# Kernel tuning notes

Measured on AMD Instinct MI355X. Metric: run time of the kernel, lower is better.

The kernel has to match this reference:

```python
import jax, jax.numpy as jnp
import numpy as np

N_NODES = 50000
N_EDGES = 600000
D = 128


def _mean_agg(h, src, dst, n_nodes):
    # DGL SAGEConv 'mean': mean of incoming src features per dst node; 0 for isolated nodes
    s = jax.ops.segment_sum(h[src], dst, num_segments=n_nodes)  # [N, d]
    deg = jax.ops.segment_sum(jnp.ones_like(dst, dtype=h.dtype), dst, num_segments=n_nodes)
    return s / jnp.maximum(deg, 1.0)[:, None]


def setup_inputs() -> dict:
    key = jax.random.key(0)
    ks = jax.random.split(key, 10)
    sc = 1.0 / np.sqrt(D)
    return {
        "x": jax.random.normal(ks[0], (N_NODES, D), jnp.float32),
        "e": jax.random.normal(ks[1], (N_EDGES, D), jnp.float32),
        "src": jax.random.randint(ks[2], (N_EDGES,), 0, N_NODES, jnp.int32),
        "dst": jax.random.randint(ks[3], (N_EDGES,), 0, N_NODES, jnp.int32),
        "W1_self": jax.random.normal(ks[4], (D, D), jnp.float32) * sc,
        "W1_neigh": jax.random.normal(ks[5], (D, D), jnp.float32) * sc,
        "b1": jnp.zeros((D,), jnp.float32),
        "W2_self": jax.random.normal(ks[6], (D, D), jnp.float32) * sc,
        "W2_neigh": jax.random.normal(ks[7], (D, D), jnp.float32) * sc,
        "b2": jnp.zeros((D,), jnp.float32),
        "Wp": jax.random.normal(ks[8], (2 * D, 3), jnp.float32) * (1.0 / np.sqrt(2 * D)),
        "bp": jnp.zeros((3,), jnp.float32),
    }


def reference(x, e, src, dst, W1_self, W1_neigh, b1, W2_self, W2_neigh, b2, Wp, bp):
    n = x.shape[0]
    # SAGEConv 1 (mean) + ReLU
    agg1 = _mean_agg(x, src, dst, n)
    h = jax.nn.relu(x @ W1_self + agg1 @ W1_neigh + b1)
    # SAGEConv 2 (mean)
    agg2 = _mean_agg(h, src, dst, n)
    h = h @ W2_self + agg2 @ W2_neigh + b2
    # MLPPredictor: per-edge gather, concat, linear (edge feature e unused in score)
    he = jnp.concatenate([h[src], h[dst]], axis=1)  # [E, 2D]
    score = he @ Wp + bp  # [E, 3]
    return score
```

## Files before the change

kernel.cpp:

```cpp
#include <hip/hip_runtime.h>
#include <hip/hip_bf16.h>


typedef __attribute__((ext_vector_type(8))) short bf16x8;
typedef __attribute__((ext_vector_type(4))) float f32x4;

static __device__ __forceinline__ float bf16lo(unsigned u) {
    return __uint_as_float(u << 16);
}
static __device__ __forceinline__ float bf16hi(unsigned u) {
    return __uint_as_float(u & 0xffff0000u);
}
static __device__ __forceinline__ unsigned short f2bf(float f) {
    unsigned u = __float_as_uint(f);
    unsigned r = 0x7fffu + ((u >> 16) & 1u);
    return (unsigned short)((u + r) >> 16);
}
static __device__ __forceinline__ unsigned pack_bf162(float a, float b) {
    return (unsigned)f2bf(a) | ((unsigned)f2bf(b) << 16);
}

#define SORT_BLOCKS 256

__global__ __launch_bounds__(256) void k_misc(
    const float* __restrict__ x, unsigned short* __restrict__ xb,
    const int* __restrict__ dst, int* __restrict__ H,
    const float* __restrict__ W1s, const float* __restrict__ W1n,
    unsigned short* __restrict__ Wt1,
    const float* __restrict__ W2s, const float* __restrict__ W2n,
    const float* __restrict__ Wp, const float* __restrict__ b2,
    const float* __restrict__ bp, float* __restrict__ Wc,
    float* __restrict__ bconst, int N, int E, int CHUNK)
{
    const int nCvt = (N * 32 + 255) / 256;
    const int b = blockIdx.x;
    const int t = threadIdx.x;

    if (b < nCvt) {
        int i = b * 256 + t;
        if (i < N * 32) {
            float4 v = ((const float4*)x)[i];
            uint2 o;
            o.x = pack_bf162(v.x, v.y);
            o.y = pack_bf162(v.z, v.w);
            *(uint2*)(xb + (size_t)i * 4) = o;
        }
    } else if (b < nCvt + SORT_BLOCKS) {
        __shared__ int hist[256];
        hist[t] = 0;
        __syncthreads();
        int blk = b - nCvt;
        int start = blk * CHUNK;
        int end = min(start + CHUNK, E);
        for (int e = start + t; e < end; e += 256)
            atomicAdd(&hist[((unsigned)dst[e]) >> 8], 1);
        __syncthreads();
        H[blk * 256 + t] = hist[t];
    } else if (b < nCvt + SORT_BLOCKS + 128) {
        int id = (b - nCvt - SORT_BLOCKS) * 256 + t;
        int k = id >> 7, n = id & 127;
        float v = (k < 128) ? W1s[k * 128 + n] : W1n[(k - 128) * 128 + n];
        Wt1[n * 256 + k] = f2bf(v);
    } else {
        for (int id = t; id < 1539; id += 256) {
            if (id < 1536) {
                int c = id / 12, j = id % 12;
                int q = j / 3, jj = j % 3;
                const float* W2 = (q == 0 || q == 2) ? W2s : W2n;
                int wpoff = (q < 2) ? 0 : 128;
                float s = 0.f;
                for (int m = 0; m < 128; ++m)
                    s += W2[c * 128 + m] * Wp[(wpoff + m) * 3 + jj];
                Wc[c * 12 + j] = s;
            } else {
                int jj = id - 1536;
                float s = bp[jj];
                for (int m = 0; m < 128; ++m)
                    s += b2[m] * (Wp[m * 3 + jj] + Wp[(128 + m) * 3 + jj]);
                bconst[jj] = s;
            }
        }
    }
}

__global__ __launch_bounds__(256) void k_s2(int* __restrict__ H,
                                            int* __restrict__ bucketBase,
                                            int NB, int E) {
    const int t = threadIdx.x;
    int tot = 0;
    for (int blk = 0; blk < SORT_BLOCKS; ++blk) tot += H[blk * 256 + t];
    __shared__ int lt[256];
    lt[t] = tot;
    __syncthreads();
    for (int off = 1; off < 256; off <<= 1) {
        int u = (t >= off) ? lt[t - off] : 0;
        __syncthreads();
        lt[t] += u;
        __syncthreads();
    }
    int excl = lt[t] - tot;
    if (t < NB) bucketBase[t] = excl;
    if (t == 0) bucketBase[NB] = E;
    int run = excl;
    for (int blk = 0; blk < SORT_BLOCKS; ++blk) {
        int h = H[blk * 256 + t];
        H[blk * 256 + t] = run;
        run += h;
    }
}

__global__ __launch_bounds__(256) void k_s3(const int* __restrict__ src,
                                            const int* __restrict__ dst,
                                            const int* __restrict__ H,
                                            int* __restrict__ packed,
                                            int E, int CHUNK) {
    __shared__ int cur[256];
    const int t = threadIdx.x, blk = blockIdx.x;
    cur[t] = H[blk * 256 + t];
    __syncthreads();
    int start = blk * CHUNK, end = min(start + CHUNK, E);
    for (int e = start + t; e < end; e += 256) {
        int d = dst[e];
        int p = atomicAdd(&cur[((unsigned)d) >> 8], 1);
        packed[p] = (src[e] & 0xFFFF) | ((d & 255) << 16);
    }
}

__global__ __launch_bounds__(256) void k_s4(const int* __restrict__ packed,
                                            const int* __restrict__ bucketBase,
                                            int* __restrict__ eidx,
                                            int* __restrict__ cursor,
                                            float* __restrict__ fdeg,
                                            float* __restrict__ invdeg, int N) {
    const int t = threadIdx.x, b = blockIdx.x;
    const int rb = bucketBase[b], re = bucketBase[b + 1];
    __shared__ int cnt[256];
    __shared__ int lt[256];
    __shared__ int cur[256];
    cnt[t] = 0;
    __syncthreads();
    for (int i = rb + t; i < re; i += 256)
        atomicAdd(&cnt[(packed[i] >> 16) & 255], 1);
    __syncthreads();
    int v = cnt[t];
    lt[t] = v;
    __syncthreads();
    for (int off = 1; off < 256; off <<= 1) {
        int u = (t >= off) ? lt[t - off] : 0;
        __syncthreads();
        lt[t] += u;
        __syncthreads();
    }
    int excl = lt[t] - v;
    int node = b * 256 + t;
    if (node < N) {
        cursor[node] = rb + excl + v;
        fdeg[node] = (float)v;
        invdeg[node] = 1.0f / fmaxf((float)v, 1.0f);
    }
    cur[t] = rb + excl;
    __syncthreads();
    for (int i = rb + t; i < re; i += 256) {
        int p = packed[i];
        int pos = atomicAdd(&cur[(p >> 16) & 255], 1);
        eidx[pos] = p & 0xFFFF;
    }
}

__global__ __launch_bounds__(256) void k_gemm_fused(
    const unsigned short* __restrict__ xb,
    const int* __restrict__ eidx, const int* __restrict__ cursor,
    const float* __restrict__ fdeg, const float* __restrict__ invdeg,
    const unsigned short* __restrict__ Wt, const float* __restrict__ bias,
    const float* __restrict__ Wc, float* __restrict__ P, int N)
{
    __shared__ __align__(16) char sW[65536];
    __shared__ float sWc[1536];
    const int t = threadIdx.x;

#pragma unroll
    for (int i = 0; i < 16; ++i) {
        int o = (i * 256 + t) * 16;
        int n = o >> 9;
        int c = o & 511;
        int sw = (n << 9) | (c ^ ((n & 7) << 4));
        *(float4*)&sW[sw] = *(const float4*)((const char*)Wt + o);
    }
    for (int i = t; i < 1536; i += 256) sWc[i] = Wc[i];

    const int wave = t >> 6, lane = t & 63;
    const int nodeBase = blockIdx.x * 128 + wave * 32;
    const int lrow = lane & 15, lk = lane >> 4;
    const int r0 = nodeBase + lrow, r1 = nodeBase + 16 + lrow;

    union { bf16x8 v; unsigned u[4]; } afrag0[4], afrag1[4];

    {
        float agg[4][8];
#pragma unroll
        for (int ksb = 0; ksb < 4; ++ksb)
#pragma unroll
            for (int i = 0; i < 8; ++i) agg[ksb][i] = 0.f;
        if (r0 < N) {
            int d = (int)fdeg[r0], o = cursor[r0] - d;
            for (int j = 0; j < d; ++j) {
                int s = eidx[o + j];
                const unsigned short* row = xb + (size_t)s * 128 + lk * 8;
#pragma unroll
                for (int ksb = 0; ksb < 4; ++ksb) {
                    uint4 v = *(const uint4*)(row + ksb * 32);
                    agg[ksb][0] += bf16lo(v.x); agg[ksb][1] += bf16hi(v.x);
                    agg[ksb][2] += bf16lo(v.y); agg[ksb][3] += bf16hi(v.y);
                    agg[ksb][4] += bf16lo(v.z); agg[ksb][5] += bf16hi(v.z);
                    agg[ksb][6] += bf16lo(v.w); agg[ksb][7] += bf16hi(v.w);
                }
            }
            float sc = invdeg[r0];
#pragma unroll
            for (int ksb = 0; ksb < 4; ++ksb)
#pragma unroll
                for (int i = 0; i < 4; ++i)
                    afrag0[ksb].u[i] = pack_bf162(agg[ksb][2 * i] * sc,
                                                  agg[ksb][2 * i + 1] * sc);
        } else {
#pragma unroll
            for (int ksb = 0; ksb < 4; ++ksb)
#pragma unroll
                for (int i = 0; i < 4; ++i) afrag0[ksb].u[i] = 0u;
        }
    }
    {
        float agg[4][8];
#pragma unroll
        for (int ksb = 0; ksb < 4; ++ksb)
#pragma unroll
            for (int i = 0; i < 8; ++i) agg[ksb][i] = 0.f;
        if (r1 < N) {
            int d = (int)fdeg[r1], o = cursor[r1] - d;
            for (int j = 0; j < d; ++j) {
                int s = eidx[o + j];
                const unsigned short* row = xb + (size_t)s * 128 + lk * 8;
#pragma unroll
                for (int ksb = 0; ksb < 4; ++ksb) {
                    uint4 v = *(const uint4*)(row + ksb * 32);
                    agg[ksb][0] += bf16lo(v.x); agg[ksb][1] += bf16hi(v.x);
                    agg[ksb][2] += bf16lo(v.y); agg[ksb][3] += bf16hi(v.y);
                    agg[ksb][4] += bf16lo(v.z); agg[ksb][5] += bf16hi(v.z);
                    agg[ksb][6] += bf16lo(v.w); agg[ksb][7] += bf16hi(v.w);
                }
            }
            float sc = invdeg[r1];
#pragma unroll
            for (int ksb = 0; ksb < 4; ++ksb)
#pragma unroll
                for (int i = 0; i < 4; ++i)
                    afrag1[ksb].u[i] = pack_bf162(agg[ksb][2 * i] * sc,
                                                  agg[ksb][2 * i + 1] * sc);
        } else {
#pragma unroll
            for (int ksb = 0; ksb < 4; ++ksb)
#pragma unroll
                for (int i = 0; i < 4; ++i) afrag1[ksb].u[i] = 0u;
        }
    }

    f32x4 acc[2][8];
#pragma unroll
    for (int rs = 0; rs < 2; ++rs)
#pragma unroll
        for (int nb = 0; nb < 8; ++nb) acc[rs][nb] = (f32x4){0.f, 0.f, 0.f, 0.f};

    __syncthreads();

    for (int ks = 0; ks < 8; ++ks) {
        bf16x8 a0, a1;
        if (ks < 4) {
            const int kk = ks * 32 + lk * 8;
            a0 = (bf16x8){};
            a1 = (bf16x8){};
            if (r0 < N) a0 = *(const bf16x8*)(xb + (size_t)r0 * 128 + kk);
            if (r1 < N) a1 = *(const bf16x8*)(xb + (size_t)r1 * 128 + kk);
        } else {
            a0 = afrag0[ks - 4].v;
            a1 = afrag1[ks - 4].v;
        }
        const int cbase = ks * 64 + lk * 16;
#pragma unroll
        for (int nb = 0; nb < 8; ++nb) {
            int n = nb * 16 + lrow;
            int sw = (n << 9) | (cbase ^ ((n & 7) << 4));
            bf16x8 b = *(const bf16x8*)&sW[sw];
            acc[0][nb] = __builtin_amdgcn_mfma_f32_16x16x32_bf16(a0, b, acc[0][nb], 0, 0, 0);
            acc[1][nb] = __builtin_amdgcn_mfma_f32_16x16x32_bf16(a1, b, acc[1][nb], 0, 0, 0);
        }
    }

#pragma unroll
    for (int rs = 0; rs < 2; ++rs) {
        float hval[8][4];
#pragma unroll
        for (int nb = 0; nb < 8; ++nb) {
            float bv = bias[nb * 16 + lrow];
#pragma unroll
            for (int r = 0; r < 4; ++r)
                hval[nb][r] = fmaxf(acc[rs][nb][r] + bv, 0.f);
        }
#pragma unroll
        for (int r = 0; r < 4; ++r) {
            float pj[12];
#pragma unroll
            for (int j = 0; j < 12; ++j) pj[j] = 0.f;
#pragma unroll
            for (int nb = 0; nb < 8; ++nb) {
                float hv = hval[nb][r];
                const float* wrow = &sWc[(nb * 16 + lrow) * 12];
#pragma unroll
                for (int j = 0; j < 12; ++j) pj[j] += hv * wrow[j];
            }
#pragma unroll
            for (int off = 8; off; off >>= 1) {
#pragma unroll
                for (int j = 0; j < 12; ++j) pj[j] += __shfl_xor(pj[j], off, 64);
            }
            int node = nodeBase + rs * 16 + lk * 4 + r;
            if (lrow == 0 && node < N) {
                float* prow = &P[(size_t)node * 16];
                *(float4*)(prow + 0) = make_float4(pj[0], pj[1], pj[2], pj[3]);
                *(float4*)(prow + 4) = make_float4(pj[4], pj[5], pj[6], pj[7]);
                *(float4*)(prow + 8) = make_float4(pj[8], pj[9], pj[10], pj[11]);
            }
        }
    }
}

__global__ __launch_bounds__(256) void k_agg3(const float* __restrict__ P,
                                              const int* __restrict__ eidx,
                                              const int* __restrict__ cursor,
                                              const float* __restrict__ fdeg,
                                              const float* __restrict__ invdeg,
                                              float* __restrict__ ps4,
                                              float* __restrict__ pd4, int N) {
    int g = (blockIdx.x * blockDim.x + threadIdx.x) >> 3;
    int j = threadIdx.x & 7;
    if (g >= N || j >= 6) return;
    int d = (int)fdeg[g];
    int o = cursor[g] - d;
    int col = (j < 3) ? (3 + j) : (6 + j);
    float a = 0.f;
    for (int i = 0; i < d; ++i) {
        int s = eidx[o + i];
        a += P[(size_t)s * 16 + col];
    }
    a *= invdeg[g];
    if (j < 3)
        ps4[(size_t)g * 4 + j] = P[(size_t)g * 16 + j] + a;
    else
        pd4[(size_t)g * 4 + (j - 3)] = P[(size_t)g * 16 + 3 + j] + a;
}

__global__ void k_edge(const float4* __restrict__ ps4, const float4* __restrict__ pd4,
                       const int* __restrict__ src, const int* __restrict__ dst,
                       const float* __restrict__ bconst, float* __restrict__ out, int E)
{
    int e = blockIdx.x * blockDim.x + threadIdx.x;
    if (e >= E) return;
    float4 a = ps4[src[e]];
    float4 b = pd4[dst[e]];
    out[(size_t)e * 3 + 0] = a.x + b.x + bconst[0];
    out[(size_t)e * 3 + 1] = a.y + b.y + bconst[1];
    out[(size_t)e * 3 + 2] = a.z + b.z + bconst[2];
}

extern "C" void kernel_launch(void* const* d_in, const int* in_sizes, int n_in,
                              void* d_out, int out_size, void* d_ws, size_t ws_size,
                              hipStream_t stream)
{
    const float* x   = (const float*)d_in[0];
    const int*   src = (const int*)d_in[2];
    const int*   dst = (const int*)d_in[3];
    const float* W1s = (const float*)d_in[4];
    const float* W1n = (const float*)d_in[5];
    const float* b1  = (const float*)d_in[6];
    const float* W2s = (const float*)d_in[7];
    const float* W2n = (const float*)d_in[8];
    const float* b2  = (const float*)d_in[9];
    const float* Wp  = (const float*)d_in[10];
    const float* bp  = (const float*)d_in[11];
    const int N = in_sizes[0] / 128;
    const int E = in_sizes[2];
    float* out = (float*)d_out;

    const int NB = (N + 255) / 256;
    const int CHUNK = (E + SORT_BLOCKS - 1) / SORT_BLOCKS;

    char* wsp = (char*)d_ws;
    auto alloc = [&](size_t bytes) { char* p = wsp; wsp += (bytes + 255) & ~(size_t)255; return p; };
    float* fdeg     = (float*)alloc((size_t)N * 4);
    float* invdeg   = (float*)alloc((size_t)N * 4);
    int*   cursor   = (int*)alloc((size_t)N * 4);
    int*   eidx     = (int*)alloc((size_t)E * 4);
    int*   packed   = (int*)alloc((size_t)E * 4);
    int*   H        = (int*)alloc((size_t)SORT_BLOCKS * 256 * 4);
    int*   bucketBase = (int*)alloc(260 * 4);
    unsigned short* xb  = (unsigned short*)alloc((size_t)N * 128 * 2);
    unsigned short* Wt1 = (unsigned short*)alloc(256 * 128 * 2);
    float* Wc     = (float*)alloc(1536 * 4);
    float* bconst = (float*)alloc(256);
    float* P      = (float*)alloc((size_t)N * 16 * 4);
    float* ps4    = (float*)alloc((size_t)N * 16);
    float* pd4    = (float*)alloc((size_t)N * 16);

    const int nCvt = (N * 32 + 255) / 256;
    k_misc<<<nCvt + SORT_BLOCKS + 129, 256, 0, stream>>>(
        x, xb, dst, H, W1s, W1n, Wt1, W2s, W2n, Wp, b2, bp, Wc, bconst, N, E, CHUNK);

    k_s2<<<1, 256, 0, stream>>>(H, bucketBase, NB, E);
    k_s3<<<SORT_BLOCKS, 256, 0, stream>>>(src, dst, H, packed, E, CHUNK);
    k_s4<<<NB, 256, 0, stream>>>(packed, bucketBase, eidx, cursor, fdeg, invdeg, N);

    k_gemm_fused<<<(N + 127) / 128, 256, 0, stream>>>(xb, eidx, cursor, fdeg, invdeg,
                                                      Wt1, b1, Wc, P, N);

    k_agg3<<<(N * 8 + 255) / 256, 256, 0, stream>>>(P, eidx, cursor, fdeg, invdeg,
                                                    ps4, pd4, N);

    k_edge<<<(E + 255) / 256, 256, 0, stream>>>((const float4*)ps4, (const float4*)pd4,
                                                src, dst, bconst, out, E);
}
```

Baseline: 174.1 us.

## Stage block edge indices in LDS, unroll gathers, and repack P columns

```diff
diff --git a/kernel.cpp b/kernel.cpp
--- a/kernel.cpp
+++ b/kernel.cpp
@@ -20,7 +20,7 @@
     return (unsigned)f2bf(a) | ((unsigned)f2bf(b) << 16);
 }
 
-#define SORT_BLOCKS 256
+#define SORT_BLOCKS 128
 
 __global__ __launch_bounds__(256) void k_misc(
     const float* __restrict__ x, unsigned short* __restrict__ xb,
@@ -177,7 +177,99 @@
     __shared__ __align__(16) char sW[65536];
     __shared__ float sWc[1536];
     const int t = threadIdx.x;
-
+    const int wave = t >> 6, lane = t & 63;
+    const int nodeBase = blockIdx.x * 128 + wave * 32;
+    const int lrow = lane & 15, lk = lane >> 4;
+    const int r0 = nodeBase + lrow, r1 = nodeBase + 16 + lrow;
+
+    int* eidxL = (int*)sW;
+    const int nb0 = blockIdx.x * 128;
+    const int lastN = min(nb0 + 127, N - 1);
+    const int estart = cursor[nb0] - (int)fdeg[nb0];
+    const int eend = cursor[lastN];
+    const int ecnt = eend - estart;
+    const bool ldsOK = (ecnt <= 16384);
+    if (ldsOK) {
+        for (int i = t; i < ecnt; i += 256) eidxL[i] = eidx[estart + i];
+    }
+    __syncthreads();
+
+    union { bf16x8 v; unsigned u[4]; } afrag0[4], afrag1[4];
+
+#define GATHER_NODE(R, EP, OFF, AF)                                          \
+    {                                                                        \
+        float agg[4][8];                                                     \
+        _Pragma("unroll") for (int ksb = 0; ksb < 4; ++ksb)                  \
+            _Pragma("unroll") for (int i = 0; i < 8; ++i) agg[ksb][i] = 0.f; \
+        if ((R) < N) {                                                       \
+            int d = (int)fdeg[R];                                            \
+            int o = (OFF);                                                   \
+            int j = 0;                                                       \
+            for (; j + 2 <= d; j += 2) {                                     \
+                int s0 = (EP)[o + j], s1 = (EP)[o + j + 1];                  \
+                const unsigned short* row0 = xb + (size_t)s0 * 128 + lk * 8; \
+                const unsigned short* row1 = xb + (size_t)s1 * 128 + lk * 8; \
+                uint4 v0[4], v1[4];                                          \
+                _Pragma("unroll") for (int ksb = 0; ksb < 4; ++ksb) {        \
+                    v0[ksb] = *(const uint4*)(row0 + ksb * 32);              \
+                    v1[ksb] = *(const uint4*)(row1 + ksb * 32);              \
+                }                                                            \
+                _Pragma("unroll") for (int ksb = 0; ksb < 4; ++ksb) {        \
+                    agg[ksb][0] += bf16lo(v0[ksb].x);                        \
+                    agg[ksb][1] += bf16hi(v0[ksb].x);                        \
+                    agg[ksb][2] += bf16lo(v0[ksb].y);                        \
+                    agg[ksb][3] += bf16hi(v0[ksb].y);                        \
+                    agg[ksb][4] += bf16lo(v0[ksb].z);                        \
+                    agg[ksb][5] += bf16hi(v0[ksb].z);                        \
+                    agg[ksb][6] += bf16lo(v0[ksb].w);                        \
+                    agg[ksb][7] += bf16hi(v0[ksb].w);                        \
+                    agg[ksb][0] += bf16lo(v1[ksb].x);                        \
+                    agg[ksb][1] += bf16hi(v1[ksb].x);                        \
+                    agg[ksb][2] += bf16lo(v1[ksb].y);                        \
+                    agg[ksb][3] += bf16hi(v1[ksb].y);                        \
+                    agg[ksb][4] += bf16lo(v1[ksb].z);                        \
+                    agg[ksb][5] += bf16hi(v1[ksb].z);                        \
+                    agg[ksb][6] += bf16lo(v1[ksb].w);                        \
+                    agg[ksb][7] += bf16hi(v1[ksb].w);                        \
+                }                                                            \
+            }                                                                \
+            if (j < d) {                                                     \
+                int s0 = (EP)[o + j];                                        \
+                const unsigned short* row0 = xb + (size_t)s0 * 128 + lk * 8; \
+                _Pragma("unroll") for (int ksb = 0; ksb < 4; ++ksb) {        \
+                    uint4 v0 = *(const uint4*)(row0 + ksb * 32);             \
+                    agg[ksb][0] += bf16lo(v0.x);                             \
+                    agg[ksb][1] += bf16hi(v0.x);                             \
+                    agg[ksb][2] += bf16lo(v0.y);                             \
+                    agg[ksb][3] += bf16hi(v0.y);                             \
+                    agg[ksb][4] += bf16lo(v0.z);                             \
+                    agg[ksb][5] += bf16hi(v0.z);                             \
+                    agg[ksb][6] += bf16lo(v0.w);                             \
+                    agg[ksb][7] += bf16hi(v0.w);                             \
+                }                                                            \
+            }                                                                \
+            float sc = invdeg[R];                                            \
+            _Pragma("unroll") for (int ksb = 0; ksb < 4; ++ksb)              \
+                _Pragma("unroll") for (int i = 0; i < 4; ++i)                \
+                    AF[ksb].u[i] = pack_bf162(agg[ksb][2 * i] * sc,          \
+                                              agg[ksb][2 * i + 1] * sc);     \
+        } else {                                                             \
+            _Pragma("unroll") for (int ksb = 0; ksb < 4; ++ksb)              \
+                _Pragma("unroll") for (int i = 0; i < 4; ++i)                \
+                    AF[ksb].u[i] = 0u;                                       \
+        }                                                                    \
+    }
+
+    if (ldsOK) {
+        GATHER_NODE(r0, eidxL, (r0 < N ? cursor[r0] - (int)fdeg[r0] - estart : 0), afrag0)
+        GATHER_NODE(r1, eidxL, (r1 < N ? cursor[r1] - (int)fdeg[r1] - estart : 0), afrag1)
+    } else {
+        GATHER_NODE(r0, eidx, (r0 < N ? cursor[r0] - (int)fdeg[r0] : 0), afrag0)
+        GATHER_NODE(r1, eidx, (r1 < N ? cursor[r1] - (int)fdeg[r1] : 0), afrag1)
+    }
+#undef GATHER_NODE
+
+    __syncthreads();
 #pragma unroll
     for (int i = 0; i < 16; ++i) {
         int o = (i * 256 + t) * 16;
@@ -187,82 +279,6 @@
         *(float4*)&sW[sw] = *(const float4*)((const char*)Wt + o);
     }
     for (int i = t; i < 1536; i += 256) sWc[i] = Wc[i];
-
-    const int wave = t >> 6, lane = t & 63;
-    const int nodeBase = blockIdx.x * 128 + wave * 32;
-    const int lrow = lane & 15, lk = lane >> 4;
-    const int r0 = nodeBase + lrow, r1 = nodeBase + 16 + lrow;
-
-    union { bf16x8 v; unsigned u[4]; } afrag0[4], afrag1[4];
-
-    {
-        float agg[4][8];
-#pragma unroll
-        for (int ksb = 0; ksb < 4; ++ksb)
-#pragma unroll
-            for (int i = 0; i < 8; ++i) agg[ksb][i] = 0.f;
-        if (r0 < N) {
-            int d = (int)fdeg[r0], o = cursor[r0] - d;
-            for (int j = 0; j < d; ++j) {
-                int s = eidx[o + j];
-                const unsigned short* row = xb + (size_t)s * 128 + lk * 8;
-#pragma unroll
-                for (int ksb = 0; ksb < 4; ++ksb) {
-                    uint4 v = *(const uint4*)(row + ksb * 32);
-                    agg[ksb][0] += bf16lo(v.x); agg[ksb][1] += bf16hi(v.x);
-                    agg[ksb][2] += bf16lo(v.y); agg[ksb][3] += bf16hi(v.y);
-                    agg[ksb][4] += bf16lo(v.z); agg[ksb][5] += bf16hi(v.z);
-                    agg[ksb][6] += bf16lo(v.w); agg[ksb][7] += bf16hi(v.w);
-                }
-            }
-            float sc = invdeg[r0];
-#pragma unroll
-            for (int ksb = 0; ksb < 4; ++ksb)
-#pragma unroll
-                for (int i = 0; i < 4; ++i)
-                    afrag0[ksb].u[i] = pack_bf162(agg[ksb][2 * i] * sc,
-                                                  agg[ksb][2 * i + 1] * sc);
-        } else {
-#pragma unroll
-            for (int ksb = 0; ksb < 4; ++ksb)
-#pragma unroll
-                for (int i = 0; i < 4; ++i) afrag0[ksb].u[i] = 0u;
-        }
-    }
-    {
-        float agg[4][8];
-#pragma unroll
-        for (int ksb = 0; ksb < 4; ++ksb)
-#pragma unroll
-            for (int i = 0; i < 8; ++i) agg[ksb][i] = 0.f;
-        if (r1 < N) {
-            int d = (int)fdeg[r1], o = cursor[r1] - d;
-            for (int j = 0; j < d; ++j) {
-                int s = eidx[o + j];
-                const unsigned short* row = xb + (size_t)s * 128 + lk * 8;
-#pragma unroll
-                for (int ksb = 0; ksb < 4; ++ksb) {
-                    uint4 v = *(const uint4*)(row + ksb * 32);
-                    agg[ksb][0] += bf16lo(v.x); agg[ksb][1] += bf16hi(v.x);
-                    agg[ksb][2] += bf16lo(v.y); agg[ksb][3] += bf16hi(v.y);
-                    agg[ksb][4] += bf16lo(v.z); agg[ksb][5] += bf16hi(v.z);
-                    agg[ksb][6] += bf16lo(v.w); agg[ksb][7] += bf16hi(v.w);
-                }
-            }
-            float sc = invdeg[r1];
-#pragma unroll
-            for (int ksb = 0; ksb < 4; ++ksb)
-#pragma unroll
-                for (int i = 0; i < 4; ++i)
-                    afrag1[ksb].u[i] = pack_bf162(agg[ksb][2 * i] * sc,
-                                                  agg[ksb][2 * i + 1] * sc);
-        } else {
-#pragma unroll
-            for (int ksb = 0; ksb < 4; ++ksb)
-#pragma unroll
-                for (int i = 0; i < 4; ++i) afrag1[ksb].u[i] = 0u;
-        }
-    }
 
     f32x4 acc[2][8];
 #pragma unroll
@@ -325,9 +341,10 @@
             int node = nodeBase + rs * 16 + lk * 4 + r;
             if (lrow == 0 && node < N) {
                 float* prow = &P[(size_t)node * 16];
-                *(float4*)(prow + 0) = make_float4(pj[0], pj[1], pj[2], pj[3]);
-                *(float4*)(prow + 4) = make_float4(pj[4], pj[5], pj[6], pj[7]);
-                *(float4*)(prow + 8) = make_float4(pj[8], pj[9], pj[10], pj[11]);
+                *(float4*)(prow + 0)  = make_float4(pj[0], pj[1], pj[2], pj[6]);
+                *(float4*)(prow + 4)  = make_float4(pj[7], pj[8], 0.f, 0.f);
+                *(float4*)(prow + 8)  = make_float4(pj[3], pj[4], pj[5], pj[9]);
+                *(float4*)(prow + 12) = make_float4(pj[10], pj[11], 0.f, 0.f);
             }
         }
     }
@@ -345,17 +362,20 @@
     if (g >= N || j >= 6) return;
     int d = (int)fdeg[g];
     int o = cursor[g] - d;
-    int col = (j < 3) ? (3 + j) : (6 + j);
     float a = 0.f;
-    for (int i = 0; i < d; ++i) {
-        int s = eidx[o + i];
-        a += P[(size_t)s * 16 + col];
-    }
+    int i = 0;
+    for (; i + 2 <= d; i += 2) {
+        int s0 = eidx[o + i], s1 = eidx[o + i + 1];
+        a += P[(size_t)s0 * 16 + 8 + j];
+        a += P[(size_t)s1 * 16 + 8 + j];
+    }
+    if (i < d) a += P[(size_t)eidx[o + i] * 16 + 8 + j];
     a *= invdeg[g];
+    float r = P[(size_t)g * 16 + j] + a;
     if (j < 3)
-        ps4[(size_t)g * 4 + j] = P[(size_t)g * 16 + j] + a;
+        ps4[(size_t)g * 4 + j] = r;
     else
-        pd4[(size_t)g * 4 + (j - 3)] = P[(size_t)g * 16 + 3 + j] + a;
+        pd4[(size_t)g * 4 + (j - 3)] = r;
 }
 
 __global__ void k_edge(const float4* __restrict__ ps4, const float4* __restrict__ pd4,
```

Result: faster. 161.4 us (-7.3%).
